# Kernel optimization log

Hardware: AMD Instinct MI355X
Metric: run time of the kernel (lower is better)

The kernel has to match this reference:

```python
import jax, jax.numpy as jnp
import numpy as np

N, IN_CH, OUT_CH = 2, 16, 32
SPATIAL = (20, 20, 20, 20)
KER = (3, 3, 3, 3)


def setup_inputs() -> dict:
    key = jax.random.key(0)
    kx, kw = jax.random.split(key)
    x = jax.random.normal(kx, (N, IN_CH) + SPATIAL, dtype=jnp.float32)
    # kaiming-uniform-like init scale; exact init distribution irrelevant for correctness baseline
    fan_in = IN_CH * int(np.prod(KER))
    bound = float(np.sqrt(6.0 / fan_in))
    w = jax.random.uniform(kw, (IN_CH, OUT_CH) + KER, dtype=jnp.float32,
                           minval=-bound, maxval=bound)
    return {"x": x, "w": w}


def reference(x, w):
    # x: [n, in_ch, d1, d2, d3, d4]; w: [in_ch, out_ch, k1, k2, k3, k4]
    # valid 4D convolution (cross-correlation), stride 1 -- same math as the
    # torch as_strided im2col + tensordot, but expressed as a sum over the
    # (small, fixed) kernel offsets to avoid materializing the im2col tensor.
    kd = w.shape[2:]
    od = tuple(x.shape[2 + i] - kd[i] + 1 for i in range(4))  # output spatial dims
    out = jnp.zeros((x.shape[0], w.shape[1]) + od, dtype=x.dtype)
    for a in range(kd[0]):
        for b in range(kd[1]):
            for c in range(kd[2]):
                for d in range(kd[3]):
                    patch = x[:, :, a:a + od[0], b:b + od[1], c:c + od[2], d:d + od[3]]
                    out = out + jnp.einsum('ncijkl,co->noijkl', patch, w[:, :, a, b, c, d])
    return out
```

## Files before the change

### kernel.cpp

```cpp
#include <hip/hip_runtime.h>


typedef unsigned short ushort_t;
typedef __attribute__((ext_vector_type(8)))  __bf16 bf16x8;
typedef __attribute__((ext_vector_type(16))) float  f32x16;
typedef __attribute__((ext_vector_type(4)))  unsigned int uint4v;

__device__ __forceinline__ ushort_t f2bf(float f) {
    union { float f; unsigned int u; } v; v.f = f;
    unsigned int r = v.u + 0x7FFFu + ((v.u >> 16) & 1u);
    return (ushort_t)(r >> 16);
}

__global__ __launch_bounds__(256) void prepass(const float* __restrict__ x,
                                               const float* __restrict__ w,
                                               ushort_t* __restrict__ xt,
                                               ushort_t* __restrict__ wt) {
    const int blk = blockIdx.x;
    if (blk < 1250) {
        const int g = blk * 256 + threadIdx.x;
        const int n = g / 160000, rem = g % 160000;
        const float* xs = x + (size_t)n * 2560000 + rem;
        unsigned int pk[8];
        #pragma unroll
        for (int e = 0; e < 8; ++e) {
            unsigned int lo = f2bf(xs[(size_t)(2 * e) * 160000]);
            unsigned int hi = f2bf(xs[(size_t)(2 * e + 1) * 160000]);
            pk[e] = lo | (hi << 16);
        }
        uint4v* q = (uint4v*)xt + (size_t)g * 2;
        uint4v q0; q0[0] = pk[0]; q0[1] = pk[1]; q0[2] = pk[2]; q0[3] = pk[3];
        uint4v q1; q1[0] = pk[4]; q1[1] = pk[5]; q1[2] = pk[6]; q1[3] = pk[7];
        q[0] = q0; q[1] = q1;
    } else {
        const int s = (blk - 1250) * 256 + threadIdx.x;
        if (s < 41472) {
            const int ic = s / 2592, rem = s % 2592;
            const int oc = rem / 81, tap = rem % 81;
            wt[tap * 512 + oc * 16 + ic] = f2bf(w[s]);
        }
    }
}

__global__ __launch_bounds__(256, 2) void conv4d_mfma(
    const ushort_t* __restrict__ xt, const ushort_t* __restrict__ wt,
    float* __restrict__ out)
{
    __shared__ ushort_t lx[2][6400];
    __shared__ float edgebuf[4][3][2][16];

    const int i = blockIdx.x, j = blockIdx.y, n = blockIdx.z;
    const int t = threadIdx.x;
    const int lane = t & 63, wv = t >> 6;
    const int col = lane & 31, ic8 = lane >> 5;

    int sp[3];
    #pragma unroll
    for (int m = 0; m < 3; ++m) sp[m] = (3 * wv + m) * 32 + col;

    f32x16 acc[3][3];
    #pragma unroll
    for (int d = 0; d < 3; ++d)
        #pragma unroll
        for (int m = 0; m < 3; ++m)
            #pragma unroll
            for (int r = 0; r < 16; ++r) acc[d][m][r] = 0.0f;

    const ushort_t* xbase = xt + (size_t)n * 2560000;

    uint4v stg[4];
    {
        const uint4v* s4 = (const uint4v*)(xbase + (size_t)i * 128000 + (size_t)j * 6400);
        stg[0] = s4[t]; stg[1] = s4[t + 256]; stg[2] = s4[t + 512];
        if (t < 32) stg[3] = s4[t + 768];
        uint4v* d4 = (uint4v*)lx[0];
        d4[t] = stg[0]; d4[t + 256] = stg[1]; d4[t + 512] = stg[2];
        if (t < 32) d4[t + 768] = stg[3];
    }

    int cur = 0;
    for (int ab = 0; ab < 9; ++ab) {
        __syncthreads();

        if (ab < 8) {
            const int a = (ab + 1) / 3, b = (ab + 1) % 3;
            const uint4v* s4 = (const uint4v*)(xbase + (size_t)(i + a) * 128000 + (size_t)(j + b) * 6400);
            stg[0] = s4[t]; stg[1] = s4[t + 256]; stg[2] = s4[t + 512];
            if (t < 32) stg[3] = s4[t + 768];
        }

        bf16x8 af[9];
        const ushort_t* wtb = wt + (ab * 9) * 512 + col * 16 + ic8 * 8;
        #pragma unroll
        for (int cd = 0; cd < 9; ++cd)
            af[cd] = *(const bf16x8*)(wtb + cd * 512);

        const char* lbase = (const char*)lx[cur];
        #pragma unroll
        for (int c = 0; c < 3; ++c) {
            #pragma unroll
            for (int m = 0; m < 3; ++m) {
                int spos = sp[m] + c * 20;
                spos = spos > 399 ? 399 : spos;
                bf16x8 bv = *(const bf16x8*)(lbase + spos * 32 + ic8 * 16);
                #pragma unroll
                for (int d = 0; d < 3; ++d)
                    acc[d][m] = __builtin_amdgcn_mfma_f32_32x32x16_bf16(af[c * 3 + d], bv, acc[d][m], 0, 0, 0);
            }
        }

        if (ab < 8) {
            uint4v* d4 = (uint4v*)lx[cur ^ 1];
            d4[t] = stg[0]; d4[t + 256] = stg[1]; d4[t + 512] = stg[2];
            if (t < 32) d4[t + 768] = stg[3];
            cur ^= 1;
        }
    }

    if (col == 0) {
        #pragma unroll
        for (int r = 0; r < 16; ++r) {
            edgebuf[wv][0][ic8][r] = acc[1][0][r];
            edgebuf[wv][1][ic8][r] = acc[2][0][r];
        }
    } else if (col == 1) {
        #pragma unroll
        for (int r = 0; r < 16; ++r)
            edgebuf[wv][2][ic8][r] = acc[2][0][r];
    }
    __syncthreads();
    const int nw = wv < 3 ? wv + 1 : 3;

    bool valm[3]; float* po[3];
    float* outn = out + (size_t)n * 3359232 + (size_t)i * 5832 + (size_t)j * 324
                      + (size_t)ic8 * 419904;
    #pragma unroll
    for (int m = 0; m < 3; ++m) {
        const int s = sp[m];
        const int k = s / 20, ls = s % 20;
        valm[m] = (ls <= 17) && (s <= 359);
        po[m] = outn + k * 18 + ls;
    }
    const int src1 = (lane & 32) | ((col + 1) & 31);
    const int src2 = (lane & 32) | ((col + 2) & 31);

    #pragma unroll
    for (int r = 0; r < 16; ++r) {
        const float e1  = edgebuf[nw][0][ic8][r];
        const float e2a = edgebuf[nw][1][ic8][r];
        const float e2b = edgebuf[nw][2][ic8][r];
        float t1[4], t2[4];
        #pragma unroll
        for (int m = 0; m < 3; ++m) {
            t1[m] = __shfl(acc[1][m][r], src1, 64);
            t2[m] = __shfl(acc[2][m][r], src2, 64);
        }
        t1[3] = e1;
        t2[3] = (col == 30) ? e2a : e2b;
        const int offr = ((r & 3) + 8 * (r >> 2)) * 104976;
        #pragma unroll
        for (int m = 0; m < 3; ++m) {
            const float v1 = (col == 31) ? t1[m + 1] : t1[m];
            const float v2 = (col >= 30) ? t2[m + 1] : t2[m];
            const float res = acc[0][m][r] + v1 + v2;
            if (valm[m]) po[m][offr] = res;
        }
    }
}

extern "C" void kernel_launch(void* const* d_in, const int* in_sizes, int n_in,
                              void* d_out, int out_size, void* d_ws, size_t ws_size,
                              hipStream_t stream) {
    const float* x = (const float*)d_in[0];
    const float* w = (const float*)d_in[1];
    float* out = (float*)d_out;

    ushort_t* xt = (ushort_t*)d_ws;
    ushort_t* wt = (ushort_t*)((char*)d_ws + (size_t)10240000);

    prepass<<<dim3(1412), 256, 0, stream>>>(x, w, xt, wt);
    conv4d_mfma<<<dim3(18, 18, 2), 256, 0, stream>>>(xt, wt, out);
}
```

Before: 50.51 us.

## Fold d-tap shift into LDS addressing, drop shuffle epilogue, remap blocks

The kernel now applies the fourth-dimension kernel offset by shifting the LDS read address, so it keeps 3 accumulators instead of 9. This removes the cross-lane shuffle and edge-buffer epilogue and frees enough registers to raise launch bounds to 3 blocks per CU. Blocks use a 1D grid with a swizzled tile mapping that spreads neighbouring tiles across XCDs. The cost is three LDS reads per tap instead of one read shared across three taps, which adds LDS traffic.

```diff
diff --git a/kernel.cpp b/kernel.cpp
--- a/kernel.cpp
+++ b/kernel.cpp
@@ -42,29 +42,32 @@
     }
 }
 
-__global__ __launch_bounds__(256, 2) void conv4d_mfma(
+__global__ __launch_bounds__(256, 3) void conv4d_mfma(
     const ushort_t* __restrict__ xt, const ushort_t* __restrict__ wt,
     float* __restrict__ out)
 {
     __shared__ ushort_t lx[2][6400];
-    __shared__ float edgebuf[4][3][2][16];
 
-    const int i = blockIdx.x, j = blockIdx.y, n = blockIdx.z;
+    const int wgid = blockIdx.x;
+    const int tile_ = (wgid & 7) * 81 + (wgid >> 3);
+    const int n = tile_ / 324;
+    const int rem_ = tile_ - n * 324;
+    const int j = rem_ / 18, i = rem_ % 18;
+
     const int t = threadIdx.x;
     const int lane = t & 63, wv = t >> 6;
     const int col = lane & 31, ic8 = lane >> 5;
 
-    int sp[3];
+    int sp0 = (3 * wv + 0) * 32 + col;
+    int sp1 = (3 * wv + 1) * 32 + col;
+    int sp2 = (3 * wv + 2) * 32 + col;
+    const int cb0 = (sp0 > 357 ? 357 : sp0) * 32 + ic8 * 16;
+    const int cb1 = (sp1 > 357 ? 357 : sp1) * 32 + ic8 * 16;
+    const int cb2 = (sp2 > 357 ? 357 : sp2) * 32 + ic8 * 16;
+
+    f32x16 acc0, acc1, acc2;
     #pragma unroll
-    for (int m = 0; m < 3; ++m) sp[m] = (3 * wv + m) * 32 + col;
-
-    f32x16 acc[3][3];
-    #pragma unroll
-    for (int d = 0; d < 3; ++d)
-        #pragma unroll
-        for (int m = 0; m < 3; ++m)
-            #pragma unroll
-            for (int r = 0; r < 16; ++r) acc[d][m][r] = 0.0f;
+    for (int r = 0; r < 16; ++r) { acc0[r] = 0.0f; acc1[r] = 0.0f; acc2[r] = 0.0f; }
 
     const ushort_t* xbase = xt + (size_t)n * 2560000;
 
@@ -95,17 +98,20 @@
         for (int cd = 0; cd < 9; ++cd)
             af[cd] = *(const bf16x8*)(wtb + cd * 512);
 
-        const char* lbase = (const char*)lx[cur];
+        const char* p0 = (const char*)lx[cur] + cb0;
+        const char* p1 = (const char*)lx[cur] + cb1;
+        const char* p2 = (const char*)lx[cur] + cb2;
         #pragma unroll
         for (int c = 0; c < 3; ++c) {
             #pragma unroll
-            for (int m = 0; m < 3; ++m) {
-                int spos = sp[m] + c * 20;
-                spos = spos > 399 ? 399 : spos;
-                bf16x8 bv = *(const bf16x8*)(lbase + spos * 32 + ic8 * 16);
-                #pragma unroll
-                for (int d = 0; d < 3; ++d)
-                    acc[d][m] = __builtin_amdgcn_mfma_f32_32x32x16_bf16(af[c * 3 + d], bv, acc[d][m], 0, 0, 0);
+            for (int d = 0; d < 3; ++d) {
+                const int off = (c * 20 + d) * 32;
+                bf16x8 b0 = *(const bf16x8*)(p0 + off);
+                bf16x8 b1 = *(const bf16x8*)(p1 + off);
+                bf16x8 b2 = *(const bf16x8*)(p2 + off);
+                acc0 = __builtin_amdgcn_mfma_f32_32x32x16_bf16(af[c * 3 + d], b0, acc0, 0, 0, 0);
+                acc1 = __builtin_amdgcn_mfma_f32_32x32x16_bf16(af[c * 3 + d], b1, acc1, 0, 0, 0);
+                acc2 = __builtin_amdgcn_mfma_f32_32x32x16_bf16(af[c * 3 + d], b2, acc2, 0, 0, 0);
             }
         }
 
@@ -117,53 +123,18 @@
         }
     }
 
-    if (col == 0) {
-        #pragma unroll
-        for (int r = 0; r < 16; ++r) {
-            edgebuf[wv][0][ic8][r] = acc[1][0][r];
-            edgebuf[wv][1][ic8][r] = acc[2][0][r];
-        }
-    } else if (col == 1) {
-        #pragma unroll
-        for (int r = 0; r < 16; ++r)
-            edgebuf[wv][2][ic8][r] = acc[2][0][r];
-    }
-    __syncthreads();
-    const int nw = wv < 3 ? wv + 1 : 3;
-
-    bool valm[3]; float* po[3];
     float* outn = out + (size_t)n * 3359232 + (size_t)i * 5832 + (size_t)j * 324
                       + (size_t)ic8 * 419904;
     #pragma unroll
     for (int m = 0; m < 3; ++m) {
-        const int s = sp[m];
+        const int s = (m == 0) ? sp0 : (m == 1) ? sp1 : sp2;
+        const f32x16& am = (m == 0) ? acc0 : (m == 1) ? acc1 : acc2;
         const int k = s / 20, ls = s % 20;
-        valm[m] = (ls <= 17) && (s <= 359);
-        po[m] = outn + k * 18 + ls;
-    }
-    const int src1 = (lane & 32) | ((col + 1) & 31);
-    const int src2 = (lane & 32) | ((col + 2) & 31);
-
-    #pragma unroll
-    for (int r = 0; r < 16; ++r) {
-        const float e1  = edgebuf[nw][0][ic8][r];
-        const float e2a = edgebuf[nw][1][ic8][r];
-        const float e2b = edgebuf[nw][2][ic8][r];
-        float t1[4], t2[4];
-        #pragma unroll
-        for (int m = 0; m < 3; ++m) {
-            t1[m] = __shfl(acc[1][m][r], src1, 64);
-            t2[m] = __shfl(acc[2][m][r], src2, 64);
-        }
-        t1[3] = e1;
-        t2[3] = (col == 30) ? e2a : e2b;
-        const int offr = ((r & 3) + 8 * (r >> 2)) * 104976;
-        #pragma unroll
-        for (int m = 0; m < 3; ++m) {
-            const float v1 = (col == 31) ? t1[m + 1] : t1[m];
-            const float v2 = (col >= 30) ? t2[m + 1] : t2[m];
-            const float res = acc[0][m][r] + v1 + v2;
-            if (valm[m]) po[m][offr] = res;
+        if (ls <= 17 && s <= 357) {
+            float* po = outn + k * 18 + ls;
+            #pragma unroll
+            for (int r = 0; r < 16; ++r)
+                po[(size_t)(((r & 3) + 8 * (r >> 2)) * 104976)] = am[r];
         }
     }
 }
@@ -179,5 +150,5 @@
     ushort_t* wt = (ushort_t*)((char*)d_ws + (size_t)10240000);
 
     prepass<<<dim3(1412), 256, 0, stream>>>(x, w, xt, wt);
-    conv4d_mfma<<<dim3(18, 18, 2), 256, 0, stream>>>(xt, wt, out);
+    conv4d_mfma<<<dim3(648), 256, 0, stream>>>(xt, wt, out);
 }
```

Measured after the change: 47.67 us. 1.06x faster.
